# Optimization experiments

Measured on AMD Instinct MI355X. Metric: run time of the kernel, lower is better.

## Reference

```python
import jax, jax.numpy as jnp
import numpy as np

D_MODEL = 1024
D_INNER = 2048
D_STATE = 16
D_CONV = 4
DT_RANK = 64
RANK = 16
LORA_SCALING = 2.0  # alpha/rank = 32/16
BATCH = 2
SEQLEN = 2048


def setup_inputs() -> dict:
    key = jax.random.key(0)
    ks = jax.random.split(key, 14)
    s = lambda i, shape, sc=1.0: jax.random.normal(ks[i], shape, dtype=jnp.float32) * sc
    return {
        "x": s(0, (BATCH, SEQLEN, D_MODEL)),
        # adapted in_proj (base Linear bias=False + masked LoRA)
        "w_in": s(1, (2 * D_INNER, D_MODEL), 0.02),
        "lora_A_in": s(2, (RANK, D_MODEL), 0.01),
        "lora_B_in": s(3, (2 * D_INNER, RANK), 0.01),
        "mask_in": jnp.ones((2 * D_INNER,), jnp.float32),
        # depthwise causal conv1d
        "conv_w": s(4, (D_INNER, 1, D_CONV), 0.1),
        "conv_b": s(5, (D_INNER,), 0.1),
        # x_proj (bias=False) and dt_proj
        "w_xproj": s(6, (DT_RANK + 2 * D_STATE, D_INNER), 0.02),
        "w_dt": s(7, (D_INNER, DT_RANK), 0.02),
        "b_dt": s(8, (D_INNER,), 0.1),
        # SSM params (S4D-real init for A_log)
        "A_log": jnp.log(jnp.tile(jnp.arange(1, D_STATE + 1, dtype=jnp.float32), (D_INNER, 1))),
        "Dp": s(9, (D_INNER,), 0.1) + 1.0,
        # adapted out_proj
        "w_out": s(10, (D_MODEL, D_INNER), 0.02),
        "lora_A_out": s(11, (RANK, D_INNER), 0.01),
        "lora_B_out": s(12, (D_MODEL, RANK), 0.01),
        "mask_out": jnp.ones((D_MODEL,), jnp.float32),
    }


def _lora_linear(x, w, a, b, mask, scaling):
    # base Linear (bias=False) + sparsity-masked LoRA update
    base = x @ w.T
    lora = ((x @ a.T) @ b.T) * mask * scaling
    return base + lora


def _selective_scan(u, delta, A, Bm, Cm, Dp):
    # u, delta: [B,L,D]; Bm, Cm: [B,L,N]; A: [D,N]; Dp: [D]
    def step(h, inp):
        d_t, b_t, c_t, u_t = inp  # [B,D], [B,N], [B,N], [B,D]
        dA = jnp.exp(d_t[..., None] * A)                     # [B,D,N]
        h = dA * h + (d_t * u_t)[..., None] * b_t[:, None, :]
        y = jnp.sum(h * c_t[:, None, :], axis=-1)            # [B,D]
        return h, y

    Bsz, L, Dd = u.shape
    h0 = jnp.zeros((Bsz, Dd, A.shape[1]), u.dtype)
    xs = (jnp.moveaxis(delta, 1, 0), jnp.moveaxis(Bm, 1, 0),
          jnp.moveaxis(Cm, 1, 0), jnp.moveaxis(u, 1, 0))
    _, ys = jax.lax.scan(step, h0, xs)
    return jnp.moveaxis(ys, 0, 1) + u * Dp


def reference(x, w_in, lora_A_in, lora_B_in, mask_in, conv_w, conv_b,
              w_xproj, w_dt, b_dt, A_log, Dp, w_out, lora_A_out,
              lora_B_out, mask_out):
    B, L, _ = x.shape
    # adapted in_proj -> [B,L,2*d_inner], split into x and gate z
    xz = _lora_linear(x, w_in, lora_A_in, lora_B_in, mask_in, LORA_SCALING)
    xs, z = jnp.split(xz, 2, axis=-1)
    # depthwise causal conv1d (torch pads d_conv-1 both sides then slices [:L])
    xc = jnp.moveaxis(xs, 1, 2)  # [B,D,L]
    xc = jax.lax.conv_general_dilated(
        xc, conv_w, window_strides=(1,), padding=[(D_CONV - 1, 0)],
        feature_group_count=D_INNER,
        dimension_numbers=("NCH", "OIH", "NCH")) + conv_b[None, :, None]
    xs = jax.nn.silu(jnp.moveaxis(xc, 1, 2))  # [B,L,D]
    # input-dependent SSM params
    x_dbl = xs @ w_xproj.T
    dt, Bm, Cm = jnp.split(x_dbl, [DT_RANK, DT_RANK + D_STATE], axis=-1)
    delta = jax.nn.softplus(dt @ w_dt.T + b_dt)  # [B,L,D]
    A = -jnp.exp(A_log)                          # [D,N]
    y = _selective_scan(xs, delta, A, Bm, Cm, Dp)
    y = y * jax.nn.silu(z)
    # adapted out_proj
    return _lora_linear(y, w_out, lora_A_out, lora_B_out, mask_out, LORA_SCALING)
```

## Files before the change

kernel.cpp:

```cpp
#include <hip/hip_runtime.h>
#include <hip/hip_bf16.h>
#include <hip/hip_fp16.h>
#include <cstdint>
#include <cstddef>

#define D_MODEL 1024
#define D_INNER 2048
#define NSTATE  16
#define DTRANK  64
#define BATCH   2
#define SEQLEN  2048
#define BL      (BATCH*SEQLEN)
#define NSEG    32
#define TSEG    (SEQLEN/NSEG)
#define SKX     8
#define KCH     (D_INNER/SKX)
#define LOG2E   1.4426950408889634f

typedef __attribute__((ext_vector_type(8))) _Float16 f16x8;
typedef __attribute__((ext_vector_type(4))) float f32x4;

__device__ __forceinline__ float softplusf(float x) {
    return fmaxf(x, 0.f) + log1pf(expf(-fabsf(x)));
}
__device__ __forceinline__ unsigned short f2h(float x) {
    __half h = __float2half(x);
    return *(unsigned short*)&h;
}
__device__ __forceinline__ void gll16(const void* g, void* l) {
    __builtin_amdgcn_global_load_lds(
        (const __attribute__((address_space(1))) void*)g,
        (__attribute__((address_space(3))) void*)l, 16, 0, 0);
}

__global__ __launch_bounds__(256) void premul_kernel(
        const float* __restrict__ lb, const float* __restrict__ mask,
        float* __restrict__ out, int total) {
    int i = blockIdx.x * 256 + threadIdx.x;
    if (i < total) out[i] = lb[i] * mask[i >> 4] * 2.0f;
}

__global__ __launch_bounds__(256) void lora_t_kernel(
        const float* __restrict__ X, int ldx,
        const float* __restrict__ LA, int K,
        float* __restrict__ T) {
    int m = blockIdx.x;
    int r = threadIdx.x >> 4;
    int l = threadIdx.x & 15;
    const float* xrow = X + (size_t)m * ldx;
    const float* arow = LA + (size_t)r * K;
    float s = 0.f;
    for (int k = 4 * l; k < K; k += 64) {
        float4 xv = *(const float4*)(xrow + k);
        float4 av = *(const float4*)(arow + k);
        s += xv.x * av.x + xv.y * av.y + xv.z * av.z + xv.w * av.w;
    }
    #pragma unroll
    for (int o = 8; o; o >>= 1) s += __shfl_xor(s, o, 16);
    if (l == 0) T[(size_t)m * 16 + r] = s;
}

__global__ __launch_bounds__(256) void cvt16_kernel(
        const float* __restrict__ src, int lda, int K4, int KP,
        unsigned short* __restrict__ dst, int total4) {
    int idx = blockIdx.x * 256 + threadIdx.x;
    if (idx >= total4) return;
    int m = idx / K4;
    int kq = idx - m * K4;
    float4 v = *(const float4*)(src + (size_t)m * lda + kq * 4);
    ushort4 h;
    h.x = f2h(v.x); h.y = f2h(v.y); h.z = f2h(v.z); h.w = f2h(v.w);
    *(ushort4*)(dst + (size_t)m * KP + kq * 4) = h;
}

__global__ __launch_bounds__(256) void cvtpad16_kernel(
        const float* __restrict__ src, int Msrc, int K4,
        unsigned short* __restrict__ dst, int total4) {
    int idx = blockIdx.x * 256 + threadIdx.x;
    if (idx >= total4) return;
    int m = idx / K4;
    int kq = idx - m * K4;
    ushort4 h = {0, 0, 0, 0};
    if (m < Msrc) {
        float4 v = *(const float4*)(src + (size_t)m * (K4 * 4) + kq * 4);
        h.x = f2h(v.x); h.y = f2h(v.y); h.z = f2h(v.z); h.w = f2h(v.w);
    }
    *(ushort4*)(dst + (size_t)m * (K4 * 4) + kq * 4) = h;
}

__global__ __launch_bounds__(256) void ext16_kernel(
        const float* __restrict__ t16, int K, int KP, int ncols,
        unsigned short* __restrict__ dst, int M) {
    int idx = blockIdx.x * 256 + threadIdx.x;
    if (idx >= M * ncols) return;
    int c = idx % ncols, m = idx / ncols;
    unsigned short hv = 0;
    if (c < 16) hv = f2h(t16[(size_t)m * 16 + c]);
    dst[(size_t)m * KP + K + c] = hv;
}

template<int EPI>
__global__ __launch_bounds__(256, 4) void mfma_gemm16(
        const unsigned short* __restrict__ Ag, const unsigned short* __restrict__ Wg,
        int KP, float* __restrict__ C, int ldc,
        const float* __restrict__ bias, int Nbound, int kchunk) {
    __shared__ __align__(16) short Ash[2][4][128][8];
    __shared__ __align__(16) short Wsh[2][4][128][8];
    const int tid = threadIdx.x;
    const int bn0 = blockIdx.x * 128, bm0 = blockIdx.y * 128;
    const int wave = tid >> 6, lane = tid & 63;
    const int wr = (wave >> 1) * 64, wc = (wave & 1) * 64;
    const int fr = lane & 15, fg = lane >> 4;
    int koff0 = 0, KT;
    if (kchunk) {
        koff0 = blockIdx.z * kchunk;
        KT = kchunk >> 5;
        C += (size_t)blockIdx.z * gridDim.y * 128 * ldc;
    } else {
        KT = KP >> 5;
    }
    const int srow = tid & 127, skg = tid >> 7;

    const unsigned short* pA = Ag + (size_t)(bm0 + srow) * KP + koff0 + skg * 8;
    const unsigned short* pW = Wg + (size_t)(bn0 + srow) * KP + koff0 + skg * 8;

    f32x4 acc[4][4];
    #pragma unroll
    for (int i = 0; i < 4; ++i)
        #pragma unroll
        for (int j = 0; j < 4; ++j) acc[i][j] = (f32x4){0.f, 0.f, 0.f, 0.f};

    auto stage = [&](int kt, int pb) {
        const int koff = kt * 32;
        gll16(pA + koff,      &Ash[pb][skg    ][srow][0]);
        gll16(pA + koff + 16, &Ash[pb][skg + 2][srow][0]);
        gll16(pW + koff,      &Wsh[pb][skg    ][srow][0]);
        gll16(pW + koff + 16, &Wsh[pb][skg + 2][srow][0]);
    };

    stage(0, 0);
    for (int kt = 0; kt < KT; ++kt) {
        const int cur = kt & 1;
        __syncthreads();
        if (kt + 1 < KT) stage(kt + 1, cur ^ 1);
        f16x8 a[4], w[4];
        #pragma unroll
        for (int i = 0; i < 4; ++i) {
            a[i] = *(const f16x8*)&Ash[cur][fg][wr + i * 16 + fr][0];
            w[i] = *(const f16x8*)&Wsh[cur][fg][wc + i * 16 + fr][0];
        }
        #pragma unroll
        for (int i = 0; i < 4; ++i)
            #pragma unroll
            for (int j = 0; j < 4; ++j)
                acc[i][j] = __builtin_amdgcn_mfma_f32_16x16x32_f16(a[i], w[j], acc[i][j], 0, 0, 0);
    }
    #pragma unroll
    for (int i = 0; i < 4; ++i) {
        #pragma unroll
        for (int j = 0; j < 4; ++j) {
            int n = bn0 + wc + j * 16 + fr;
            if (n < Nbound) {
                #pragma unroll
                for (int q = 0; q < 4; ++q) {
                    int m = bm0 + wr + i * 16 + fg * 4 + q;
                    float v = acc[i][j][q];
                    if (EPI == 2) v = softplusf(v + bias[n]);
                    C[(size_t)m * ldc + n] = v;
                }
            }
        }
    }
}

__global__ __launch_bounds__(256) void sk2_reduce_kernel(
        const float* __restrict__ p, float* __restrict__ out, int total) {
    int i = blockIdx.x * 256 + threadIdx.x;
    if (i < total) out[i] = p[i] + p[(size_t)total + i];
}

__global__ __launch_bounds__(256) void sk_reduce_kernel(
        const float* __restrict__ part, float* __restrict__ out, int total) {
    int i = blockIdx.x * 256 + threadIdx.x;
    if (i >= total) return;
    float s = 0.f;
    #pragma unroll
    for (int sk = 0; sk < SKX; ++sk) s += part[(size_t)sk * total + i];
    out[i] = s;
}

__global__ __launch_bounds__(256) void conv_silu_kernel(
        const float* __restrict__ xz, const float* __restrict__ cw,
        const float* __restrict__ cb, float* __restrict__ u,
        unsigned short* __restrict__ u16) {
    int idx = blockIdx.x * 256 + threadIdx.x;
    int d  = idx & (D_INNER - 1);
    int bl = idx >> 11;
    int l  = bl & (SEQLEN - 1);
    const float* base = xz + (size_t)bl * 4096 + d;
    float4 w = *(const float4*)(cw + d * 4);
    float s = cb[d];
    if (l >= 3) s = fmaf(base[-3 * 4096], w.x, s);
    if (l >= 2) s = fmaf(base[-2 * 4096], w.y, s);
    if (l >= 1) s = fmaf(base[-1 * 4096], w.z, s);
    s = fmaf(base[0], w.w, s);
    float r = s * __builtin_amdgcn_rcpf(1.f + __expf(-s));
    u[idx] = r;
    u16[idx] = f2h(r);
}

__global__ __launch_bounds__(256) void scan_partA(
        const float* __restrict__ delta, const float* __restrict__ u,
        const float* __restrict__ xdbl, const float* __restrict__ A_log,
        float* __restrict__ hF, float* __restrict__ sumd) {
    const int tid = threadIdx.x;
    const int bx  = blockIdx.x;
    const int seg = bx >> 4;
    const int b   = (bx >> 3) & 1;
    const int d   = (bx & 7) * 256 + tid;
    const int t0  = seg * TSEG;
    float An2[16];
    #pragma unroll
    for (int q = 0; q < 4; ++q) {
        float4 a = *(const float4*)(A_log + d * 16 + q * 4);
        An2[q*4+0] = -__expf(a.x) * LOG2E;
        An2[q*4+1] = -__expf(a.y) * LOG2E;
        An2[q*4+2] = -__expf(a.z) * LOG2E;
        An2[q*4+3] = -__expf(a.w) * LOG2E;
    }
    const float* dl = delta + ((size_t)b * SEQLEN + t0) * D_INNER + d;
    const float* uu = u     + ((size_t)b * SEQLEN + t0) * D_INNER + d;
    const float* bc = xdbl  + ((size_t)b * SEQLEN + t0) * 96 + 64;
    float h[16];
    #pragma unroll
    for (int n = 0; n < 16; ++n) h[n] = 0.f;
    float sd = 0.f;
    float pdv[4], puv[4];
    #pragma unroll
    for (int j = 0; j < 4; ++j) {
        pdv[j] = dl[(size_t)j * D_INNER];
        puv[j] = uu[(size_t)j * D_INNER];
    }
    for (int t4 = 0; t4 < TSEG; t4 += 4) {
        #pragma unroll
        for (int j = 0; j < 4; ++j) {
            const float dv = pdv[j], uv = puv[j];
            if (t4 + 4 < TSEG) {
                pdv[j] = dl[(size_t)(t4 + 4 + j) * D_INNER];
                puv[j] = uu[(size_t)(t4 + 4 + j) * D_INNER];
            }
            const float* bct = bc + (size_t)(t4 + j) * 96;
            float4 B0 = *(const float4*)(bct);
            float4 B1 = *(const float4*)(bct + 4);
            float4 B2 = *(const float4*)(bct + 8);
            float4 B3 = *(const float4*)(bct + 12);
            float Bv[16] = {B0.x,B0.y,B0.z,B0.w, B1.x,B1.y,B1.z,B1.w,
                            B2.x,B2.y,B2.z,B2.w, B3.x,B3.y,B3.z,B3.w};
            const float dvuv = dv * uv;
            sd += dv;
            #pragma unroll
            for (int n = 0; n < 16; ++n)
                h[n] = fmaf(exp2f(dv * An2[n]), h[n], dvuv * Bv[n]);
        }
    }
    const size_t o = (size_t)seg * (BATCH * D_INNER) + (size_t)b * D_INNER + d;
    #pragma unroll
    for (int q = 0; q < 4; ++q)
        *(float4*)(hF + o * 16 + q * 4) =
            make_float4(h[q*4], h[q*4+1], h[q*4+2], h[q*4+3]);
    sumd[o] = sd;
}

__global__ __launch_bounds__(256) void scan_combine(
        const float* __restrict__ A_log, float* __restrict__ hFin,
        const float* __restrict__ sumd) {
    int idx = blockIdx.x * 256 + threadIdx.x;
    int n = idx & 15, row = idx >> 4;
    int d = row & (D_INNER - 1);
    float An = -__expf(A_log[d * 16 + n]);
    float f[NSEG], p[NSEG];
    #pragma unroll
    for (int s = 0; s < NSEG; ++s) {
        size_t o = (size_t)s * (BATCH * D_INNER) + row;
        f[s] = hFin[o * 16 + n];
        p[s] = __expf(An * sumd[o]);
    }
    float h = 0.f;
    #pragma unroll
    for (int s = 0; s < NSEG; ++s) {
        size_t o = (size_t)s * (BATCH * D_INNER) + row;
        hFin[o * 16 + n] = h;
        h = fmaf(p[s], h, f[s]);
    }
}

__global__ __launch_bounds__(256) void scan_partB(
        const float* delta, const float* __restrict__ u,
        const float* __restrict__ xdbl, const float* __restrict__ xz,
        const float* __restrict__ A_log, const float* __restrict__ Dp,
        const float* __restrict__ hin, float* yg) {
    const int tid = threadIdx.x;
    const int bx  = blockIdx.x;
    const int seg = bx >> 4;
    const int b   = (bx >> 3) & 1;
    const int d   = (bx & 7) * 256 + tid;
    const int t0  = seg * TSEG;
    float An2[16];
    #pragma unroll
    for (int q = 0; q < 4; ++q) {
        float4 a = *(const float4*)(A_log + d * 16 + q * 4);
        An2[q*4+0] = -__expf(a.x) * LOG2E;
        An2[q*4+1] = -__expf(a.y) * LOG2E;
        An2[q*4+2] = -__expf(a.z) * LOG2E;
        An2[q*4+3] = -__expf(a.w) * LOG2E;
    }
    const float Dd = Dp[d];
    const float* dl = delta + ((size_t)b * SEQLEN + t0) * D_INNER + d;
    const float* uu = u     + ((size_t)b * SEQLEN + t0) * D_INNER + d;
    const float* bc = xdbl  + ((size_t)b * SEQLEN + t0) * 96 + 64;
    const float* zz = xz    + ((size_t)b * SEQLEN + t0) * 4096 + D_INNER + d;
    float* yo = yg + ((size_t)b * SEQLEN + t0) * D_INNER + d;
    const size_t o = (size_t)seg * (BATCH * D_INNER) + (size_t)b * D_INNER + d;
    float h[16];
    #pragma unroll
    for (int q = 0; q < 4; ++q) {
        float4 hv = *(const float4*)(hin + o * 16 + q * 4);
        h[q*4] = hv.x; h[q*4+1] = hv.y; h[q*4+2] = hv.z; h[q*4+3] = hv.w;
    }
    float pdv[4], puv[4], pzv[4];
    #pragma unroll
    for (int j = 0; j < 4; ++j) {
        pdv[j] = dl[(size_t)j * D_INNER];
        puv[j] = uu[(size_t)j * D_INNER];
        pzv[j] = zz[(size_t)j * 4096];
    }
    for (int t4 = 0; t4 < TSEG; t4 += 4) {
        #pragma unroll
        for (int j = 0; j < 4; ++j) {
            const float dv = pdv[j], uv = puv[j], zv = pzv[j];
            if (t4 + 4 < TSEG) {
                pdv[j] = dl[(size_t)(t4 + 4 + j) * D_INNER];
                puv[j] = uu[(size_t)(t4 + 4 + j) * D_INNER];
                pzv[j] = zz[(size_t)(t4 + 4 + j) * 4096];
            }
            const float* bct = bc + (size_t)(t4 + j) * 96;
            float4 B0 = *(const float4*)(bct);
            float4 B1 = *(const float4*)(bct + 4);
            float4 B2 = *(const float4*)(bct + 8);
            float4 B3 = *(const float4*)(bct + 12);
            float4 C0 = *(const float4*)(bct + 16);
            float4 C1 = *(const float4*)(bct + 20);
            float4 C2 = *(const float4*)(bct + 24);
            float4 C3 = *(const float4*)(bct + 28);
            float Bv[16] = {B0.x,B0.y,B0.z,B0.w, B1.x,B1.y,B1.z,B1.w,
                            B2.x,B2.y,B2.z,B2.w, B3.x,B3.y,B3.z,B3.w};
            float Cv[16] = {C0.x,C0.y,C0.z,C0.w, C1.x,C1.y,C1.z,C1.w,
                            C2.x,C2.y,C2.z,C2.w, C3.x,C3.y,C3.z,C3.w};
            const float dvuv = dv * uv;
            #pragma unroll
            for (int n = 0; n < 16; ++n)
                h[n] = fmaf(exp2f(dv * An2[n]), h[n], dvuv * Bv[n]);
            float acc[4] = {0.f, 0.f, 0.f, 0.f};
            #pragma unroll
            for (int n = 0; n < 16; ++n)
                acc[n & 3] = fmaf(h[n], Cv[n], acc[n & 3]);
            float yv = fmaf(uv, Dd, (acc[0] + acc[1]) + (acc[2] + acc[3]));
            float sig = zv * __builtin_amdgcn_rcpf(1.f + __expf(-zv));
            yo[(size_t)(t4 + j) * D_INNER] = yv * sig;
        }
    }
}

extern "C" void kernel_launch(void* const* d_in, const int* in_sizes, int n_in,
                              void* d_out, int out_size, void* d_ws, size_t ws_size,
                              hipStream_t stream) {
    const float* x        = (const float*)d_in[0];
    const float* w_in     = (const float*)d_in[1];
    const float* lA_in    = (const float*)d_in[2];
    const float* lB_in    = (const float*)d_in[3];
    const float* mask_in  = (const float*)d_in[4];
    const float* conv_w   = (const float*)d_in[5];
    const float* conv_b   = (const float*)d_in[6];
    const float* w_xp     = (const float*)d_in[7];
    const float* w_dt     = (const float*)d_in[8];
    const float* b_dt     = (const float*)d_in[9];
    const float* A_log    = (const float*)d_in[10];
    const float* Dp       = (const float*)d_in[11];
    const float* w_out    = (const float*)d_in[12];
    const float* lA_out   = (const float*)d_in[13];
    const float* lB_out   = (const float*)d_in[14];
    const float* mask_out = (const float*)d_in[15];

    float* ws    = (float*)d_ws;
    float* xz    = ws;
    float* u     = xz    + (size_t)BL * 4096;
    float* delta = u     + (size_t)BL * D_INNER;
    float* xdbl  = delta + (size_t)BL * D_INNER;
    float* t16   = xdbl  + (size_t)BL * 96;
    float* lbin  = t16   + (size_t)BL * 16;
    float* lbout = lbin  + (size_t)4096 * 16;

    unsigned short* A16_in = (unsigned short*)u;
    unsigned short* W16_in = A16_in + (size_t)4096 * 1056;

    unsigned short* u16 = (unsigned short*)delta;

    const int KP_OUT = 2112, KH_OUT = 1056;
    unsigned short* A16_out = (unsigned short*)xz;
    unsigned short* W16_out = A16_out + (size_t)4096 * KP_OUT;

    float* outf    = (float*)d_out;
    float* xp_part = outf;
    unsigned short* W16_xp = (unsigned short*)(outf + (size_t)SKX * BL * 96);
    unsigned short* A16_dt = (unsigned short*)d_out;
    unsigned short* W16_dt = A16_dt + (size_t)4096 * 64;
    float* hFin    = outf;
    float* sumd    = hFin + (size_t)NSEG * BATCH * D_INNER * 16;

    premul_kernel<<<(4096 * 16 + 255) / 256, 256, 0, stream>>>(lB_in, mask_in, lbin, 4096 * 16);
    premul_kernel<<<(1024 * 16 + 255) / 256, 256, 0, stream>>>(lB_out, mask_out, lbout, 1024 * 16);
    lora_t_kernel<<<BL, 256, 0, stream>>>(x, D_MODEL, lA_in, D_MODEL, t16);
    cvt16_kernel<<<4096, 256, 0, stream>>>(x,    1024, 256, 1056, A16_in, 4096 * 256);
    cvt16_kernel<<<4096, 256, 0, stream>>>(w_in, 1024, 256, 1056, W16_in, 4096 * 256);
    ext16_kernel<<<512, 256, 0, stream>>>(t16,  1024, 1056, 32, A16_in, 4096);
    ext16_kernel<<<512, 256, 0, stream>>>(lbin, 1024, 1056, 32, W16_in, 4096);
    mfma_gemm16<0><<<dim3(32, 32), 256, 0, stream>>>(
        A16_in, W16_in, 1056, xz, 4096, nullptr, 4096, 0);
    conv_silu_kernel<<<(BL * D_INNER) / 256, 256, 0, stream>>>(xz, conv_w, conv_b, u, u16);
    cvtpad16_kernel<<<(128 * 512 + 255) / 256, 256, 0, stream>>>(w_xp, 96, 512, W16_xp, 128 * 512);
    mfma_gemm16<0><<<dim3(1, 32, SKX), 256, 0, stream>>>(
        u16, W16_xp, 2048, xp_part, 96, nullptr, 96, KCH);
    sk_reduce_kernel<<<(BL * 96 + 255) / 256, 256, 0, stream>>>(xp_part, xdbl, BL * 96);
    cvt16_kernel<<<(4096 * 16 + 255) / 256, 256, 0, stream>>>(xdbl, 96, 16, 64, A16_dt, 4096 * 16);
    cvt16_kernel<<<(2048 * 16 + 255) / 256, 256, 0, stream>>>(w_dt, 64, 16, 64, W16_dt, 2048 * 16);
    mfma_gemm16<2><<<dim3(16, 32), 256, 0, stream>>>(
        A16_dt, W16_dt, 64, delta, 2048, b_dt, 2048, 0);
    scan_partA<<<NSEG * BATCH * 8, 256, 0, stream>>>(delta, u, xdbl, A_log, hFin, sumd);
    scan_combine<<<(BATCH * D_INNER * 16) / 256, 256, 0, stream>>>(A_log, hFin, sumd);
    scan_partB<<<NSEG * BATCH * 8, 256, 0, stream>>>(delta, u, xdbl, xz, A_log, Dp, hFin, delta);
    lora_t_kernel<<<BL, 256, 0, stream>>>(delta, D_INNER, lA_out, D_INNER, t16);
    cvt16_kernel<<<8192, 256, 0, stream>>>(delta, 2048, 512, KP_OUT, A16_out, 4096 * 512);
    cvt16_kernel<<<2048, 256, 0, stream>>>(w_out, 2048, 512, KP_OUT, W16_out, 1024 * 512);
    ext16_kernel<<<(4096 * 64 + 255) / 256, 256, 0, stream>>>(t16,   2048, KP_OUT, 64, A16_out, 4096);
    ext16_kernel<<<(1024 * 64 + 255) / 256, 256, 0, stream>>>(lbout, 2048, KP_OUT, 64, W16_out, 1024);
    float* P = delta;
    mfma_gemm16<0><<<dim3(8, 32, 2), 256, 0, stream>>>(
        A16_out, W16_out, KP_OUT, P, 1024, nullptr, 1024, KH_OUT);
    sk2_reduce_kernel<<<(4096 * 1024) / 256, 256, 0, stream>>>(P, (float*)d_out, 4096 * 1024);
}
```

Before: 442.8 us.

## Double scan segments, stage B/C in LDS, relocate scan state into xz

Increases the number of chunked-scan segments from 32 to 64, doubling the blocks in both scan passes so more of the GPU is busy while each block walks a shorter serial stretch. Each scan block now copies its segment's B (and C) coefficients into shared memory once, instead of every thread re-reading them from global memory at each timestep. The larger per-segment state no longer fits in the output buffer, so it is stored in the dead x-half of the xz buffer through a strided address helper. The combine kernel now walks twice as many segments with a small register prefetch, which adds serial work there, and the scan kernels gain a block-wide barrier.

Result: faster. 410.9 us (-7.2%).

```diff
diff --git a/kernel.cpp b/kernel.cpp
--- a/kernel.cpp
+++ b/kernel.cpp
@@ -11,11 +11,12 @@
 #define BATCH   2
 #define SEQLEN  2048
 #define BL      (BATCH*SEQLEN)
-#define NSEG    32
+#define NSEG    64
 #define TSEG    (SEQLEN/NSEG)
 #define SKX     8
 #define KCH     (D_INNER/SKX)
 #define LOG2E   1.4426950408889634f
+#define HF_BASE ((size_t)NSEG * BATCH * D_INNER * 16)
 
 typedef __attribute__((ext_vector_type(8))) _Float16 f16x8;
 typedef __attribute__((ext_vector_type(4))) float f32x4;
@@ -26,6 +27,12 @@
 __device__ __forceinline__ unsigned short f2h(float x) {
     __half h = __float2half(x);
     return *(unsigned short*)&h;
+}
+__device__ __forceinline__ float* hfp(float* xzb, size_t i) {
+    return xzb + (i >> 11) * 4096 + (i & 2047);
+}
+__device__ __forceinline__ const float* hfpc(const float* xzb, size_t i) {
+    return xzb + (i >> 11) * 4096 + (i & 2047);
 }
 __device__ __forceinline__ void gll16(const void* g, void* l) {
     __builtin_amdgcn_global_load_lds(
@@ -212,13 +219,19 @@
 __global__ __launch_bounds__(256) void scan_partA(
         const float* __restrict__ delta, const float* __restrict__ u,
         const float* __restrict__ xdbl, const float* __restrict__ A_log,
-        float* __restrict__ hF, float* __restrict__ sumd) {
+        float* __restrict__ xzws) {
+    __shared__ float Bs[TSEG][16];
     const int tid = threadIdx.x;
     const int bx  = blockIdx.x;
     const int seg = bx >> 4;
     const int b   = (bx >> 3) & 1;
     const int d   = (bx & 7) * 256 + tid;
     const int t0  = seg * TSEG;
+    {
+        const float* bc0 = xdbl + ((size_t)b * SEQLEN + t0) * 96 + 64;
+        for (int i = tid; i < TSEG * 16; i += 256)
+            Bs[i >> 4][i & 15] = bc0[(size_t)(i >> 4) * 96 + (i & 15)];
+    }
     float An2[16];
     #pragma unroll
     for (int q = 0; q < 4; ++q) {
@@ -230,7 +243,6 @@
     }
     const float* dl = delta + ((size_t)b * SEQLEN + t0) * D_INNER + d;
     const float* uu = u     + ((size_t)b * SEQLEN + t0) * D_INNER + d;
-    const float* bc = xdbl  + ((size_t)b * SEQLEN + t0) * 96 + 64;
     float h[16];
     #pragma unroll
     for (int n = 0; n < 16; ++n) h[n] = 0.f;
@@ -241,6 +253,7 @@
         pdv[j] = dl[(size_t)j * D_INNER];
         puv[j] = uu[(size_t)j * D_INNER];
     }
+    __syncthreads();
     for (int t4 = 0; t4 < TSEG; t4 += 4) {
         #pragma unroll
         for (int j = 0; j < 4; ++j) {
@@ -249,48 +262,53 @@
                 pdv[j] = dl[(size_t)(t4 + 4 + j) * D_INNER];
                 puv[j] = uu[(size_t)(t4 + 4 + j) * D_INNER];
             }
-            const float* bct = bc + (size_t)(t4 + j) * 96;
-            float4 B0 = *(const float4*)(bct);
-            float4 B1 = *(const float4*)(bct + 4);
-            float4 B2 = *(const float4*)(bct + 8);
-            float4 B3 = *(const float4*)(bct + 12);
-            float Bv[16] = {B0.x,B0.y,B0.z,B0.w, B1.x,B1.y,B1.z,B1.w,
-                            B2.x,B2.y,B2.z,B2.w, B3.x,B3.y,B3.z,B3.w};
             const float dvuv = dv * uv;
             sd += dv;
             #pragma unroll
             for (int n = 0; n < 16; ++n)
-                h[n] = fmaf(exp2f(dv * An2[n]), h[n], dvuv * Bv[n]);
+                h[n] = fmaf(exp2f(dv * An2[n]), h[n], dvuv * Bs[t4 + j][n]);
         }
     }
     const size_t o = (size_t)seg * (BATCH * D_INNER) + (size_t)b * D_INNER + d;
     #pragma unroll
     for (int q = 0; q < 4; ++q)
-        *(float4*)(hF + o * 16 + q * 4) =
+        *(float4*)hfp(xzws, o * 16 + q * 4) =
             make_float4(h[q*4], h[q*4+1], h[q*4+2], h[q*4+3]);
-    sumd[o] = sd;
+    *hfp(xzws, HF_BASE + o) = sd;
 }
 
 __global__ __launch_bounds__(256) void scan_combine(
-        const float* __restrict__ A_log, float* __restrict__ hFin,
-        const float* __restrict__ sumd) {
+        const float* __restrict__ A_log, float* xzws) {
     int idx = blockIdx.x * 256 + threadIdx.x;
     int n = idx & 15, row = idx >> 4;
     int d = row & (D_INNER - 1);
     float An = -__expf(A_log[d * 16 + n]);
-    float f[NSEG], p[NSEG];
-    #pragma unroll
-    for (int s = 0; s < NSEG; ++s) {
-        size_t o = (size_t)s * (BATCH * D_INNER) + row;
-        f[s] = hFin[o * 16 + n];
-        p[s] = __expf(An * sumd[o]);
-    }
     float h = 0.f;
-    #pragma unroll
-    for (int s = 0; s < NSEG; ++s) {
-        size_t o = (size_t)s * (BATCH * D_INNER) + row;
-        hFin[o * 16 + n] = h;
-        h = fmaf(p[s], h, f[s]);
+    float f[4], sdv[4];
+    #pragma unroll
+    for (int j = 0; j < 4; ++j) {
+        size_t o = (size_t)j * (BATCH * D_INNER) + row;
+        f[j]   = *hfpc(xzws, o * 16 + n);
+        sdv[j] = *hfpc(xzws, HF_BASE + o);
+    }
+    for (int s4 = 0; s4 < NSEG; s4 += 4) {
+        float nf[4], nsd[4];
+        if (s4 + 4 < NSEG) {
+            #pragma unroll
+            for (int j = 0; j < 4; ++j) {
+                size_t o = (size_t)(s4 + 4 + j) * (BATCH * D_INNER) + row;
+                nf[j]  = *hfpc(xzws, o * 16 + n);
+                nsd[j] = *hfpc(xzws, HF_BASE + o);
+            }
+        }
+        #pragma unroll
+        for (int j = 0; j < 4; ++j) {
+            size_t o = (size_t)(s4 + j) * (BATCH * D_INNER) + row;
+            *hfp(xzws, o * 16 + n) = h;
+            h = fmaf(__expf(An * sdv[j]), h, f[j]);
+        }
+        #pragma unroll
+        for (int j = 0; j < 4; ++j) { f[j] = nf[j]; sdv[j] = nsd[j]; }
     }
 }
 
@@ -298,13 +316,19 @@
         const float* delta, const float* __restrict__ u,
         const float* __restrict__ xdbl, const float* __restrict__ xz,
         const float* __restrict__ A_log, const float* __restrict__ Dp,
-        const float* __restrict__ hin, float* yg) {
+        float* yg) {
+    __shared__ float BCs[TSEG][32];
     const int tid = threadIdx.x;
     const int bx  = blockIdx.x;
     const int seg = bx >> 4;
     const int b   = (bx >> 3) & 1;
     const int d   = (bx & 7) * 256 + tid;
     const int t0  = seg * TSEG;
+    {
+        const float* bc0 = xdbl + ((size_t)b * SEQLEN + t0) * 96 + 64;
+        for (int i = tid; i < TSEG * 32; i += 256)
+            BCs[i >> 5][i & 31] = bc0[(size_t)(i >> 5) * 96 + (i & 31)];
+    }
     float An2[16];
     #pragma unroll
     for (int q = 0; q < 4; ++q) {
@@ -317,14 +341,13 @@
     const float Dd = Dp[d];
     const float* dl = delta + ((size_t)b * SEQLEN + t0) * D_INNER + d;
     const float* uu = u     + ((size_t)b * SEQLEN + t0) * D_INNER + d;
-    const float* bc = xdbl  + ((size_t)b * SEQLEN + t0) * 96 + 64;
     const float* zz = xz    + ((size_t)b * SEQLEN + t0) * 4096 + D_INNER + d;
     float* yo = yg + ((size_t)b * SEQLEN + t0) * D_INNER + d;
     const size_t o = (size_t)seg * (BATCH * D_INNER) + (size_t)b * D_INNER + d;
     float h[16];
     #pragma unroll
     for (int q = 0; q < 4; ++q) {
-        float4 hv = *(const float4*)(hin + o * 16 + q * 4);
+        float4 hv = *(const float4*)hfpc(xz, o * 16 + q * 4);
         h[q*4] = hv.x; h[q*4+1] = hv.y; h[q*4+2] = hv.z; h[q*4+3] = hv.w;
     }
     float pdv[4], puv[4], pzv[4];
@@ -334,6 +357,7 @@
         puv[j] = uu[(size_t)j * D_INNER];
         pzv[j] = zz[(size_t)j * 4096];
     }
+    __syncthreads();
     for (int t4 = 0; t4 < TSEG; t4 += 4) {
         #pragma unroll
         for (int j = 0; j < 4; ++j) {
@@ -343,27 +367,14 @@
                 puv[j] = uu[(size_t)(t4 + 4 + j) * D_INNER];
                 pzv[j] = zz[(size_t)(t4 + 4 + j) * 4096];
             }
-            const float* bct = bc + (size_t)(t4 + j) * 96;
-            float4 B0 = *(const float4*)(bct);
-            float4 B1 = *(const float4*)(bct + 4);
-            float4 B2 = *(const float4*)(bct + 8);
-            float4 B3 = *(const float4*)(bct + 12);
-            float4 C0 = *(const float4*)(bct + 16);
-            float4 C1 = *(const float4*)(bct + 20);
-            float4 C2 = *(const float4*)(bct + 24);
-            float4 C3 = *(const float4*)(bct + 28);
-            float Bv[16] = {B0.x,B0.y,B0.z,B0.w, B1.x,B1.y,B1.z,B1.w,
-                            B2.x,B2.y,B2.z,B2.w, B3.x,B3.y,B3.z,B3.w};
-            float Cv[16] = {C0.x,C0.y,C0.z,C0.w, C1.x,C1.y,C1.z,C1.w,
-                            C2.x,C2.y,C2.z,C2.w, C3.x,C3.y,C3.z,C3.w};
             const float dvuv = dv * uv;
             #pragma unroll
             for (int n = 0; n < 16; ++n)
-                h[n] = fmaf(exp2f(dv * An2[n]), h[n], dvuv * Bv[n]);
+                h[n] = fmaf(exp2f(dv * An2[n]), h[n], dvuv * BCs[t4 + j][n]);
             float acc[4] = {0.f, 0.f, 0.f, 0.f};
             #pragma unroll
             for (int n = 0; n < 16; ++n)
-                acc[n & 3] = fmaf(h[n], Cv[n], acc[n & 3]);
+                acc[n & 3] = fmaf(h[n], BCs[t4 + j][16 + n], acc[n & 3]);
             float yv = fmaf(uv, Dd, (acc[0] + acc[1]) + (acc[2] + acc[3]));
             float sig = zv * __builtin_amdgcn_rcpf(1.f + __expf(-zv));
             yo[(size_t)(t4 + j) * D_INNER] = yv * sig;
@@ -414,8 +425,6 @@
     unsigned short* W16_xp = (unsigned short*)(outf + (size_t)SKX * BL * 96);
     unsigned short* A16_dt = (unsigned short*)d_out;
     unsigned short* W16_dt = A16_dt + (size_t)4096 * 64;
-    float* hFin    = outf;
-    float* sumd    = hFin + (size_t)NSEG * BATCH * D_INNER * 16;
 
     premul_kernel<<<(4096 * 16 + 255) / 256, 256, 0, stream>>>(lB_in, mask_in, lbin, 4096 * 16);
     premul_kernel<<<(1024 * 16 + 255) / 256, 256, 0, stream>>>(lB_out, mask_out, lbout, 1024 * 16);
@@ -435,9 +444,9 @@
     cvt16_kernel<<<(2048 * 16 + 255) / 256, 256, 0, stream>>>(w_dt, 64, 16, 64, W16_dt, 2048 * 16);
     mfma_gemm16<2><<<dim3(16, 32), 256, 0, stream>>>(
         A16_dt, W16_dt, 64, delta, 2048, b_dt, 2048, 0);
-    scan_partA<<<NSEG * BATCH * 8, 256, 0, stream>>>(delta, u, xdbl, A_log, hFin, sumd);
-    scan_combine<<<(BATCH * D_INNER * 16) / 256, 256, 0, stream>>>(A_log, hFin, sumd);
-    scan_partB<<<NSEG * BATCH * 8, 256, 0, stream>>>(delta, u, xdbl, xz, A_log, Dp, hFin, delta);
+    scan_partA<<<NSEG * BATCH * 8, 256, 0, stream>>>(delta, u, xdbl, A_log, xz);
+    scan_combine<<<(BATCH * D_INNER * 16) / 256, 256, 0, stream>>>(A_log, xz);
+    scan_partB<<<NSEG * BATCH * 8, 256, 0, stream>>>(delta, u, xdbl, xz, A_log, Dp, delta);
     lora_t_kernel<<<BL, 256, 0, stream>>>(delta, D_INNER, lA_out, D_INNER, t16);
     cvt16_kernel<<<8192, 256, 0, stream>>>(delta, 2048, 512, KP_OUT, A16_out, 4096 * 512);
     cvt16_kernel<<<2048, 256, 0, stream>>>(w_out, 2048, 512, KP_OUT, W16_out, 1024 * 512);
```
